# Performance work log

Measured on AMD Instinct MI355X. Metric: run time of the kernel, lower is better.

Reference implementation:

```python
import jax, jax.numpy as jnp
import numpy as np

CLAMP_MIN, CLAMP_MAX = 1e-7, 10.0


def _hyper_layer(H, edge_nodes, W, b, power):
    """One HyperTensorGraphConvolution forward.

    H:          [N, d] node signals
    edge_nodes: [E, k] int node indices per hyperedge (k-1 < num_sample, so
                the sampling branch of the original code never triggers and the
                aggregation is the full power-mean over the k-1 neighbors)
    """
    H = jnp.clip(H, CLAMP_MIN, CLAMP_MAX)          # torch.clamp_(H, ...)
    inv_p = 1.0 / power
    Hp = H ** power                                 # [N, d]
    gathered = Hp[edge_nodes]                       # [E, k, d]
    edge_sum = gathered.sum(axis=1, keepdims=True)  # [E, 1, d]
    k = edge_nodes.shape[1]
    # power-mean of the other (k-1) nodes in the hyperedge, per incidence
    contrib = ((edge_sum - gathered) / (k - 1)) ** inv_p   # [E, k, d]
    # new_signal = H.clone(); scatter-add contributions per (edge, node)
    d = H.shape[1]
    new_signal = H.at[edge_nodes.reshape(-1)].add(contrib.reshape(-1, d))
    # row-normalize (rowsum^-1, inf -> 0)
    rowsum = new_signal.sum(axis=1, keepdims=True)
    r_inv = jnp.where(rowsum != 0, 1.0 / rowsum, 0.0)
    AH = new_signal * r_inv
    return AH @ W + b


def setup_inputs() -> dict:
    key = jax.random.key(0)
    k_x, k_e, k_w1, k_b1, k_w2, k_b2 = jax.random.split(key, 6)
    N, d, E, k, c = 100000, 128, 25000, 32, 40
    x = jax.random.uniform(k_x, (N, d), dtype=jnp.float32)
    edge_nodes = jax.random.randint(k_e, (E, k), 0, N, dtype=jnp.int64)
    std1 = 1.0 / np.sqrt(16.0)
    W1 = jax.random.uniform(k_w1, (d, 16), jnp.float32, -std1, std1)
    b1 = jax.random.uniform(k_b1, (16,), jnp.float32, -std1, std1)
    std2 = 1.0 / np.sqrt(float(c))
    W2 = jax.random.uniform(k_w2, (16, c), jnp.float32, -std2, std2)
    b2 = jax.random.uniform(k_b2, (c,), jnp.float32, -std2, std2)
    return {"x": x, "edge_nodes": edge_nodes, "W1": W1, "b1": b1,
            "W2": W2, "b2": b2, "power": 2}


def reference(x, edge_nodes, W1, b1, W2, b2, power):
    H = jax.nn.relu(_hyper_layer(x, edge_nodes, W1, b1, float(power)))
    # dropout is identity at inference
    out = _hyper_layer(H, edge_nodes, W2, b2, float(power))
    return out
```

## Files before the change

### kernel.cpp

```cpp
#include <hip/hip_runtime.h>
#include <hip/hip_fp16.h>
#include <math.h>

#define CAP 64
#define L16 16
#define OVF 48
#define D1 128
#define D2 16
#define C_OUT 40
#define K_EDGE 32
#define CLAMP_LO 1e-7f
#define CLAMP_HI 10.0f
#define SQRT_INV31 0.1796053020267749f

typedef unsigned short ushort_t;
typedef _Float16 hv2 __attribute__((ext_vector_type(2)));

__device__ __forceinline__ hv2 hv2_zero() {
    hv2 z; z.x = (_Float16)0; z.y = (_Float16)0; return z;
}

__global__ __launch_bounds__(256) void k_setup(const float* __restrict__ x,
                                               hv2* __restrict__ Hp,
                                               const int* __restrict__ idx,
                                               int* __restrict__ deg,
                                               ushort_t* __restrict__ lst,
                                               ushort_t* __restrict__ ovf,
                                               const float* __restrict__ W1,
                                               float* __restrict__ W1t,
                                               hv2* __restrict__ S,
                                               float* __restrict__ S2,
                                               int n4, int total, int E) {
    int i = blockIdx.x * 256 + threadIdx.x;
    if (i < n4) {
        float4 v = ((const float4*)x)[i];
        v.x = fminf(fmaxf(v.x, CLAMP_LO), CLAMP_HI);
        v.y = fminf(fmaxf(v.y, CLAMP_LO), CLAMP_HI);
        v.z = fminf(fmaxf(v.z, CLAMP_LO), CLAMP_HI);
        v.w = fminf(fmaxf(v.w, CLAMP_LO), CLAMP_HI);
        hv2 h0; h0.x = (_Float16)(v.x * v.x); h0.y = (_Float16)(v.y * v.y);
        hv2 h1; h1.x = (_Float16)(v.z * v.z); h1.y = (_Float16)(v.w * v.w);
        Hp[2 * i] = h0; Hp[2 * i + 1] = h1;
    }
    if (i < total) {
        int n = idx[i];
        int e = i >> 5;
        int pos = atomicAdd(&deg[n], 1);
        if (pos < L16)      lst[n * L16 + pos] = (ushort_t)e;
        else if (pos < CAP) ovf[n * OVF + (pos - L16)] = (ushort_t)e;
    }
    if (i < D1 * D2) W1t[(i & 15) * D1 + (i >> 4)] = W1[i];
    if (i < 64) S[(size_t)E * 64 + i] = hv2_zero();
    if (i < D2) S2[(size_t)E * D2 + i] = 0.0f;
}

__global__ __launch_bounds__(256) void k_edge_sum(const hv2* __restrict__ Hp,
                                                  const int* __restrict__ idx,
                                                  hv2* __restrict__ S, int E) {
    int w = threadIdx.x >> 6;
    int lane = threadIdx.x & 63;
    int eA = (blockIdx.x * 4 + w) * 4;
    if (eA + 4 > E) eA = E - 4;
    int nid0 = idx[eA * K_EDGE + lane];
    int nid1 = idx[eA * K_EDGE + 64 + lane];
    hv2 acc[4][2];
#pragma unroll
    for (int k = 0; k < 4; k++) { acc[k][0] = hv2_zero(); acc[k][1] = hv2_zero(); }
#pragma unroll
    for (int j = 0; j < K_EDGE; j++) {
        int g = j >> 4;
        int nA = __builtin_amdgcn_readlane(nid0, j);
        int nB = __builtin_amdgcn_readlane(nid0, 32 + j);
        int nC = __builtin_amdgcn_readlane(nid1, j);
        int nD = __builtin_amdgcn_readlane(nid1, 32 + j);
        acc[0][g] += Hp[(size_t)nA * 64 + lane];
        acc[1][g] += Hp[(size_t)nB * 64 + lane];
        acc[2][g] += Hp[(size_t)nC * 64 + lane];
        acc[3][g] += Hp[(size_t)nD * 64 + lane];
    }
#pragma unroll
    for (int k = 0; k < 4; k++)
        S[(size_t)(eA + k) * 64 + lane] = acc[k][0] + acc[k][1];
}

__global__ __launch_bounds__(256) void k_node1(const hv2* __restrict__ Hp,
                                               const hv2* __restrict__ S,
                                               const int* __restrict__ deg,
                                               const ushort_t* __restrict__ lst,
                                               const ushort_t* __restrict__ ovf,
                                               const float* __restrict__ W1t,
                                               const float* __restrict__ b1,
                                               _Float16* __restrict__ Hp2, int N, int E) {
    int w = threadIdx.x >> 6;
    int lane = threadIdx.x & 63;
    int pair = blockIdx.x * 4 + w;
    int n0 = pair * 2, n1 = n0 + 1;
    int q = lane & 15, g = lane >> 4;

    int2 dg2 = ((const int2*)deg)[pair];
    int dg0 = min(dg2.x, CAP), dg1 = min(dg2.y, CAP);
    int nodesel = (lane < 16) ? n0 : n1;
    ushort_t idu = (lane < 32) ? lst[nodesel * L16 + q] : (ushort_t)0;
    int dsel = (lane < 16) ? dg0 : dg1;
    int e_sel = (lane < 32 && q < dsel) ? (int)idu : E;

    hv2 hph0 = Hp[(size_t)n0 * 64 + lane];
    hv2 hph1 = Hp[(size_t)n1 * 64 + lane];

    hv2 sv0[16], sv1[16];
#pragma unroll
    for (int t = 0; t < 16; t++) {
        int e = __builtin_amdgcn_readlane(e_sel, t);
        sv0[t] = S[(size_t)e * 64 + lane];
    }
#pragma unroll
    for (int t = 0; t < 16; t++) {
        int e = __builtin_amdgcn_readlane(e_sel, 16 + t);
        sv1[t] = S[(size_t)e * 64 + lane];
    }

    hv2 z = hv2_zero();
    hv2 A0a = z, A0b = z, A1a = z, A1b = z;
#pragma unroll
    for (int t = 0; t < 16; t += 2) {
        hv2 d0 = __builtin_elementwise_max(sv0[t] - hph0, z);
        hv2 d1 = __builtin_elementwise_max(sv0[t + 1] - hph0, z);
        A0a += __builtin_elementwise_sqrt(d0);
        A0b += __builtin_elementwise_sqrt(d1);
    }
#pragma unroll
    for (int t = 0; t < 16; t += 2) {
        hv2 d0 = __builtin_elementwise_max(sv1[t] - hph1, z);
        hv2 d1 = __builtin_elementwise_max(sv1[t + 1] - hph1, z);
        A1a += __builtin_elementwise_sqrt(d0);
        A1b += __builtin_elementwise_sqrt(d1);
    }
    for (int t = 16; t < dg0; t++) {
        int e = ovf[n0 * OVF + (t - 16)];
        hv2 d = __builtin_elementwise_max(S[(size_t)e * 64 + lane] - hph0, z);
        A0a += __builtin_elementwise_sqrt(d);
    }
    for (int t = 16; t < dg1; t++) {
        int e = ovf[n1 * OVF + (t - 16)];
        hv2 d = __builtin_elementwise_max(S[(size_t)e * 64 + lane] - hph1, z);
        A1a += __builtin_elementwise_sqrt(d);
    }
    hv2 A0 = A0a + A0b, A1 = A1a + A1b;

    float ns00 = __builtin_amdgcn_sqrtf((float)hph0.x) + (float)A0.x * SQRT_INV31;
    float ns01 = __builtin_amdgcn_sqrtf((float)hph0.y) + (float)A0.y * SQRT_INV31;
    float ns10 = __builtin_amdgcn_sqrtf((float)hph1.x) + (float)A1.x * SQRT_INV31;
    float ns11 = __builtin_amdgcn_sqrtf((float)hph1.y) + (float)A1.y * SQRT_INV31;

    __shared__ float AHs[4][2][D1];
    AHs[w][0][2 * lane]     = ns00;
    AHs[w][0][2 * lane + 1] = ns01;
    AHs[w][1][2 * lane]     = ns10;
    AHs[w][1][2 * lane + 1] = ns11;

    float v0 = ns00 + ns01, v1 = ns10 + ns11;
#pragma unroll
    for (int m = 1; m < 64; m <<= 1) {
        v0 += __shfl_xor(v0, m, 64);
        v1 += __shfl_xor(v1, m, 64);
    }
    float r0 = __builtin_amdgcn_rcpf(v0);
    float r1 = __builtin_amdgcn_rcpf(v1);

    __threadfence_block();

    const float4* a0p = (const float4*)(&AHs[w][0][g * 32]);
    const float4* a1p = (const float4*)(&AHs[w][1][g * 32]);
    const float4* w1p = (const float4*)(W1t + q * D1 + g * 32);
    float p0 = 0.0f, p1 = 0.0f;
#pragma unroll
    for (int tt = 0; tt < 8; tt++) {
        float4 wv = w1p[tt];
        float4 x0 = a0p[tt];
        float4 x1 = a1p[tt];
        p0 += x0.x * wv.x + x0.y * wv.y + x0.z * wv.z + x0.w * wv.w;
        p1 += x1.x * wv.x + x1.y * wv.y + x1.z * wv.z + x1.w * wv.w;
    }
    p0 += __shfl_xor(p0, 16, 64);
    p0 += __shfl_xor(p0, 32, 64);
    p1 += __shfl_xor(p1, 16, 64);
    p1 += __shfl_xor(p1, 32, 64);
    if (lane < D2) {
        float bb = b1[q];
        float o0 = bb + p0 * r0;
        float o1 = bb + p1 * r1;
        float cl0 = fminf(fmaxf(o0, CLAMP_LO), CLAMP_HI);
        float cl1 = fminf(fmaxf(o1, CLAMP_LO), CLAMP_HI);
        Hp2[(size_t)n0 * D2 + q] = (_Float16)(cl0 * cl0);
        Hp2[(size_t)n1 * D2 + q] = (_Float16)(cl1 * cl1);
    }
}

__global__ __launch_bounds__(256) void k_edge_sum2(const hv2* __restrict__ Hp2v,
                                                   const int* __restrict__ idx,
                                                   float2* __restrict__ S2v, int E) {
    int w = threadIdx.x >> 6;
    int lane = threadIdx.x & 63;
    int sub = lane >> 3;
    int cp = lane & 7;
    int e = (blockIdx.x * 4 + w) * 8 + sub;
    if (e >= E) e = E - 1;
    const int* ip = idx + (size_t)e * K_EDGE;
    hv2 g0 = hv2_zero(), g1 = hv2_zero();
#pragma unroll
    for (int j = 0; j < 16; j++)  g0 += Hp2v[(size_t)ip[j] * 8 + cp];
#pragma unroll
    for (int j = 16; j < 32; j++) g1 += Hp2v[(size_t)ip[j] * 8 + cp];
    float2 s; s.x = (float)g0.x + (float)g1.x; s.y = (float)g0.y + (float)g1.y;
    S2v[(size_t)e * 8 + cp] = s;
}

__global__ __launch_bounds__(256) void k_node2(const _Float16* __restrict__ Hp2,
                                               const float* __restrict__ S2,
                                               const int* __restrict__ deg,
                                               const ushort_t* __restrict__ lst,
                                               const ushort_t* __restrict__ ovf,
                                               const float* __restrict__ W2,
                                               const float* __restrict__ b2,
                                               float* __restrict__ out, int N, int E) {
    int w = threadIdx.x >> 6;
    int lane = threadIdx.x & 63;
    int pair = blockIdx.x * 4 + w;
    int n0 = pair * 2, n1 = n0 + 1;
    int col = lane & 15;
    int node = lane >> 5;
    int gg = (lane >> 4) & 1;
    int nn = node ? n1 : n0;

    int2 dg2 = ((const int2*)deg)[pair];
    int dg0 = min(dg2.x, CAP), dg1 = min(dg2.y, CAP);
    int sl = lane & 15;
    ushort_t idu = (lane < 32) ? lst[((lane < 16) ? n0 : n1) * L16 + sl] : (ushort_t)0;
    int dsel = (lane < 16) ? dg0 : dg1;
    int e_sel = (lane < 32 && sl < dsel) ? (int)idu : E;

    float hp = (float)Hp2[(size_t)nn * D2 + col];
    int dgn = node ? dg1 : dg0;

    int ev[8];
#pragma unroll
    for (int t = 0; t < 8; t++) ev[t] = __shfl(e_sel, node * 16 + 2 * t + gg, 64);
    float sv[8];
#pragma unroll
    for (int t = 0; t < 8; t++) sv[t] = S2[(size_t)ev[t] * D2 + col];

    float acc = 0.0f;
#pragma unroll
    for (int t = 0; t < 8; t++)
        acc += __builtin_amdgcn_sqrtf(fmaxf(sv[t] - hp, 0.0f));
    for (int t = 16; t < dgn; t++) {
        int e = ovf[nn * OVF + (t - 16)];
        float s = S2[(size_t)e * D2 + col];
        if (gg == 0) acc += __builtin_amdgcn_sqrtf(fmaxf(s - hp, 0.0f));
    }
    acc += __shfl_xor(acc, 16, 64);
    float ns = __builtin_amdgcn_sqrtf(hp) + acc * SQRT_INV31;

    float v = ns;
#pragma unroll
    for (int m = 1; m < 16; m <<= 1) v += __shfl_xor(v, m, 64);
    float r = __builtin_amdgcn_rcpf(v);

    __shared__ float AHs[4][2][D2];
    if (gg == 0) AHs[w][node][col] = ns * r;
    __threadfence_block();

    if (lane < C_OUT) {
        float o0 = b2[lane], o1 = o0;
#pragma unroll
        for (int i = 0; i < D2; i++) {
            float wv = W2[i * C_OUT + lane];
            o0 += AHs[w][0][i] * wv;
            o1 += AHs[w][1][i] * wv;
        }
        out[(size_t)n0 * C_OUT + lane] = o0;
        out[(size_t)n1 * C_OUT + lane] = o1;
    }
}

extern "C" void kernel_launch(void* const* d_in, const int* in_sizes, int n_in,
                              void* d_out, int out_size, void* d_ws, size_t ws_size,
                              hipStream_t stream) {
    const float* x   = (const float*)d_in[0];
    const int*   idx = (const int*)d_in[1];
    const float* W1  = (const float*)d_in[2];
    const float* b1  = (const float*)d_in[3];
    const float* W2  = (const float*)d_in[4];
    const float* b2  = (const float*)d_in[5];
    float* out = (float*)d_out;

    int N = in_sizes[0] / D1;
    int E = in_sizes[1] / K_EDGE;

    hv2* Hp = (hv2*)d_ws;
    hv2* S  = Hp + (size_t)N * 64;
    _Float16* Hp2h = (_Float16*)(S + (size_t)(E + 1) * 64);
    float* S2   = (float*)(Hp2h + (size_t)N * D2);
    float* W1t  = S2 + (size_t)(E + 1) * D2;
    int*   deg  = (int*)(W1t + D1 * D2);
    ushort_t* lst = (ushort_t*)(deg + N);
    ushort_t* ovf = lst + (size_t)N * L16;

    int total = E * K_EDGE;
    int n4 = N * D1 / 4;

    (void)hipMemsetAsync(deg, 0, (size_t)N * sizeof(int), stream);
    k_setup<<<(n4 + 255) / 256, 256, 0, stream>>>(x, Hp, idx, deg, lst, ovf, W1,
                                                  W1t, S, S2, n4, total, E);
    k_edge_sum<<<(E + 15) / 16, 256, 0, stream>>>(Hp, idx, S, E);
    k_node1<<<N / 8, 256, 0, stream>>>(Hp, S, deg, lst, ovf, W1t, b1, Hp2h, N, E);
    k_edge_sum2<<<(E + 31) / 32, 256, 0, stream>>>((const hv2*)Hp2h, idx, (float2*)S2, E);
    k_node2<<<N / 8, 256, 0, stream>>>(Hp2h, S2, deg, lst, ovf, W2, b2, out, N, E);
}
```

Measured before the change: 259.7 us.

## Move incidence-list build into edge-sum kernel and use one edge per wave

```diff
diff --git a/kernel.cpp b/kernel.cpp
--- a/kernel.cpp
+++ b/kernel.cpp
@@ -22,15 +22,11 @@
 
 __global__ __launch_bounds__(256) void k_setup(const float* __restrict__ x,
                                                hv2* __restrict__ Hp,
-                                               const int* __restrict__ idx,
-                                               int* __restrict__ deg,
-                                               ushort_t* __restrict__ lst,
-                                               ushort_t* __restrict__ ovf,
                                                const float* __restrict__ W1,
                                                float* __restrict__ W1t,
                                                hv2* __restrict__ S,
                                                float* __restrict__ S2,
-                                               int n4, int total, int E) {
+                                               int n4, int E) {
     int i = blockIdx.x * 256 + threadIdx.x;
     if (i < n4) {
         float4 v = ((const float4*)x)[i];
@@ -42,45 +38,51 @@
         hv2 h1; h1.x = (_Float16)(v.z * v.z); h1.y = (_Float16)(v.w * v.w);
         Hp[2 * i] = h0; Hp[2 * i + 1] = h1;
     }
-    if (i < total) {
-        int n = idx[i];
-        int e = i >> 5;
-        int pos = atomicAdd(&deg[n], 1);
-        if (pos < L16)      lst[n * L16 + pos] = (ushort_t)e;
-        else if (pos < CAP) ovf[n * OVF + (pos - L16)] = (ushort_t)e;
-    }
     if (i < D1 * D2) W1t[(i & 15) * D1 + (i >> 4)] = W1[i];
     if (i < 64) S[(size_t)E * 64 + i] = hv2_zero();
     if (i < D2) S2[(size_t)E * D2 + i] = 0.0f;
 }
 
-__global__ __launch_bounds__(256) void k_edge_sum(const hv2* __restrict__ Hp,
-                                                  const int* __restrict__ idx,
-                                                  hv2* __restrict__ S, int E) {
+__global__ __launch_bounds__(256) void k_edge_build(const hv2* __restrict__ Hp,
+                                                    const int* __restrict__ idx,
+                                                    hv2* __restrict__ S,
+                                                    int* __restrict__ deg,
+                                                    ushort_t* __restrict__ lst,
+                                                    ushort_t* __restrict__ ovf,
+                                                    int E, int nBuild, int total4) {
+    if ((int)blockIdx.x < nBuild) {
+        int i = blockIdx.x * 256 + threadIdx.x;
+        if (i < total4) {
+            int4 nn = ((const int4*)idx)[i];
+            int p0 = atomicAdd(&deg[nn.x], 1);
+            int p1 = atomicAdd(&deg[nn.y], 1);
+            int p2 = atomicAdd(&deg[nn.z], 1);
+            int p3 = atomicAdd(&deg[nn.w], 1);
+            ushort_t e = (ushort_t)(i >> 3);
+            if (p0 < L16) lst[nn.x * L16 + p0] = e;
+            else if (p0 < CAP) ovf[nn.x * OVF + (p0 - L16)] = e;
+            if (p1 < L16) lst[nn.y * L16 + p1] = e;
+            else if (p1 < CAP) ovf[nn.y * OVF + (p1 - L16)] = e;
+            if (p2 < L16) lst[nn.z * L16 + p2] = e;
+            else if (p2 < CAP) ovf[nn.z * OVF + (p2 - L16)] = e;
+            if (p3 < L16) lst[nn.w * L16 + p3] = e;
+            else if (p3 < CAP) ovf[nn.w * OVF + (p3 - L16)] = e;
+        }
+        return;
+    }
+    int b = blockIdx.x - nBuild;
     int w = threadIdx.x >> 6;
     int lane = threadIdx.x & 63;
-    int eA = (blockIdx.x * 4 + w) * 4;
-    if (eA + 4 > E) eA = E - 4;
-    int nid0 = idx[eA * K_EDGE + lane];
-    int nid1 = idx[eA * K_EDGE + 64 + lane];
-    hv2 acc[4][2];
-#pragma unroll
-    for (int k = 0; k < 4; k++) { acc[k][0] = hv2_zero(); acc[k][1] = hv2_zero(); }
+    int e = b * 4 + w;
+    int nid = (lane < K_EDGE) ? idx[e * K_EDGE + lane] : 0;
+    hv2 accA = hv2_zero(), accB = hv2_zero();
 #pragma unroll
     for (int j = 0; j < K_EDGE; j++) {
-        int g = j >> 4;
-        int nA = __builtin_amdgcn_readlane(nid0, j);
-        int nB = __builtin_amdgcn_readlane(nid0, 32 + j);
-        int nC = __builtin_amdgcn_readlane(nid1, j);
-        int nD = __builtin_amdgcn_readlane(nid1, 32 + j);
-        acc[0][g] += Hp[(size_t)nA * 64 + lane];
-        acc[1][g] += Hp[(size_t)nB * 64 + lane];
-        acc[2][g] += Hp[(size_t)nC * 64 + lane];
-        acc[3][g] += Hp[(size_t)nD * 64 + lane];
-    }
-#pragma unroll
-    for (int k = 0; k < 4; k++)
-        S[(size_t)(eA + k) * 64 + lane] = acc[k][0] + acc[k][1];
+        int n = __builtin_amdgcn_readlane(nid, j);
+        hv2 h = Hp[(size_t)n * 64 + lane];
+        if (j < 16) accA += h; else accB += h;
+    }
+    S[(size_t)e * 64 + lane] = accA + accB;
 }
 
 __global__ __launch_bounds__(256) void k_node1(const hv2* __restrict__ Hp,
@@ -306,13 +308,14 @@
     ushort_t* lst = (ushort_t*)(deg + N);
     ushort_t* ovf = lst + (size_t)N * L16;
 
-    int total = E * K_EDGE;
+    int total4 = E * K_EDGE / 4;
+    int nBuild = (total4 + 255) / 256;
     int n4 = N * D1 / 4;
 
     (void)hipMemsetAsync(deg, 0, (size_t)N * sizeof(int), stream);
-    k_setup<<<(n4 + 255) / 256, 256, 0, stream>>>(x, Hp, idx, deg, lst, ovf, W1,
-                                                  W1t, S, S2, n4, total, E);
-    k_edge_sum<<<(E + 15) / 16, 256, 0, stream>>>(Hp, idx, S, E);
+    k_setup<<<(n4 + 255) / 256, 256, 0, stream>>>(x, Hp, W1, W1t, S, S2, n4, E);
+    k_edge_build<<<nBuild + E / 4, 256, 0, stream>>>(Hp, idx, S, deg, lst, ovf,
+                                                     E, nBuild, total4);
     k_node1<<<N / 8, 256, 0, stream>>>(Hp, S, deg, lst, ovf, W1t, b1, Hp2h, N, E);
     k_edge_sum2<<<(E + 31) / 32, 256, 0, stream>>>((const hv2*)Hp2h, idx, (float2*)S2, E);
     k_node2<<<N / 8, 256, 0, stream>>>(Hp2h, S2, deg, lst, ovf, W2, b2, out, N, E);
```

Result: no change. 261.2 us (+0.6%).
